# Kernel tuning notes

Hardware: AMD Instinct MI355X
Metric: run time of the kernel (lower is better)

## Reference

```python
import jax, jax.numpy as jnp
import numpy as np

B, S, D, H = 2, 2048, 1024, 16
HD = D // H


def setup_inputs() -> dict:
    key = jax.random.key(0)
    ks = jax.random.split(key, 6)
    scale = D ** -0.5
    return {
        "x": jax.random.normal(ks[0], (B, S, D), dtype=jnp.float32),
        "attn_mask": jnp.ones((B, S), dtype=bool),
        "wq": jax.random.normal(ks[1], (D, D), dtype=jnp.float32) * scale,
        "wk": jax.random.normal(ks[2], (D, D), dtype=jnp.float32) * scale,
        "wv": jax.random.normal(ks[3], (D, D), dtype=jnp.float32) * scale,
        "wo": jax.random.normal(ks[4], (D, D), dtype=jnp.float32) * scale,
        "bo": jax.random.normal(ks[5], (D,), dtype=jnp.float32) * 0.01,
    }


def reference(x, attn_mask, wq, wk, wv, wo, bo):
    b, s, d = x.shape
    # torch Linear: y = x @ W.T
    q = (x @ wq.T).reshape(b, s, H, HD).transpose(0, 2, 1, 3)  # (b,h,s,hd)
    k = (x @ wk.T).reshape(b, s, H, HD).transpose(0, 2, 1, 3)
    v = (x @ wv.T).reshape(b, s, H, HD).transpose(0, 2, 1, 3)
    scores = jnp.einsum("bhqd,bhkd->bhqk", q, k) * (HD ** -0.5)
    causal = jnp.triu(jnp.ones((s, s), dtype=bool), k=1)  # True above diagonal
    mask = causal[None, None, :, :] | (~attn_mask)[:, None, None, :]
    mask_value = jnp.finfo(scores.dtype).min / 2
    scores = jnp.where(mask, mask_value, scores)
    att = jax.nn.softmax(scores, axis=-1)
    ctx = jnp.einsum("bhqk,bhkd->bhqd", att, v)
    ctx = ctx.transpose(0, 2, 1, 3).reshape(b, s, d)
    return ctx @ wo.T + bo
```

## Files before the change

kernel.cpp:

```cpp
#include <hip/hip_runtime.h>
#include <stdint.h>

#define SEQ   2048
#define DMODEL 1024
#define NHEAD 16
#define HDIM  64
#define MTOT  4096

typedef short s16x8 __attribute__((ext_vector_type(8)));
typedef float f32x4 __attribute__((ext_vector_type(4)));
typedef float f32x16 __attribute__((ext_vector_type(16)));
typedef unsigned u32x4 __attribute__((ext_vector_type(4)));

#define LOG2E 1.44269504088896340736f

#if __has_builtin(__builtin_amdgcn_exp2f)
#define EXP2(x) __builtin_amdgcn_exp2f(x)
#else
#define EXP2(x) exp2f(x)
#endif

#define WAITV0 asm volatile("s_waitcnt vmcnt(0)" ::: "memory")
#define WAITV3 asm volatile("s_waitcnt vmcnt(3)" ::: "memory")
#define WAITV4 asm volatile("s_waitcnt vmcnt(4)" ::: "memory")

__device__ __forceinline__ short f2bf(float f) {
  union { float f; unsigned u; } v; v.f = f;
  unsigned u = v.u + 0x7fff + ((v.u >> 16) & 1);
  return (short)(u >> 16);
}

__device__ __forceinline__ void async_cp16(const void* g, void* l) {
  __builtin_amdgcn_global_load_lds(
      (const __attribute__((address_space(1))) void*)g,
      (__attribute__((address_space(3))) void*)l, 16, 0, 0);
}

__device__ __forceinline__ f32x4 mfma16(s16x8 a, s16x8 b, f32x4 c) {
  return __builtin_amdgcn_mfma_f32_16x16x32_bf16(a, b, c, 0, 0, 0);
}
__device__ __forceinline__ f32x16 mfma32(s16x8 a, s16x8 b, f32x16 c) {
  return __builtin_amdgcn_mfma_f32_32x32x16_bf16(a, b, c, 0, 0, 0);
}

__device__ __forceinline__ void plane32swap(unsigned& a, unsigned& b) {
#if __has_builtin(__builtin_amdgcn_permlane32_swap)
  auto r = __builtin_amdgcn_permlane32_swap(a, b, false, false);
  a = r[0]; b = r[1];
#else
  asm("v_permlane32_swap_b32 %0, %1" : "+v"(a), "+v"(b));
#endif
}

__global__ __launch_bounds__(256) void cast_kernel(
    const float* __restrict__ x,  const float* __restrict__ wq,
    const float* __restrict__ wk, const float* __restrict__ wv,
    const float* __restrict__ wo,
    short* __restrict__ xb,  short* __restrict__ wqb,
    short* __restrict__ wkb, short* __restrict__ wvb, short* __restrict__ wob) {
  int i = blockIdx.x * 256 + threadIdx.x;
  const float4* src; short* dst; int off;
  const int XN = 1 << 20, WN = 1 << 18;
  if (i < XN)            { src = (const float4*)x;  dst = xb;  off = i; }
  else if (i < XN + WN)  { src = (const float4*)wq; dst = wqb; off = i - XN; }
  else if (i < XN + 2*WN){ src = (const float4*)wk; dst = wkb; off = i - XN - WN; }
  else if (i < XN + 3*WN){ src = (const float4*)wv; dst = wvb; off = i - XN - 2*WN; }
  else                   { src = (const float4*)wo; dst = wob; off = i - XN - 3*WN; }
  float4 v = src[off];
  short4 o; o.x = f2bf(v.x); o.y = f2bf(v.y); o.z = f2bf(v.z); o.w = f2bf(v.w);
  *(short4*)(dst + off * 4) = o;
}

__global__ __launch_bounds__(512, 2) void qkv_gemm(
    const short* __restrict__ xb,  const short* __restrict__ wqb,
    const short* __restrict__ wkb, const short* __restrict__ wvb,
    short* __restrict__ Q, short* __restrict__ K, short* __restrict__ Vt) {
  __shared__ short SMEM[49152];
  short (*Abuf)[4096] = reinterpret_cast<short (*)[4096]>(SMEM);
  short (*Bbuf)[3][4096] = reinterpret_cast<short (*)[3][4096]>(SMEM + 3 * 4096);
  const int tid = threadIdx.x;
  const int w = tid >> 6, lane = tid & 63;
  const int c = lane & 15, g = lane >> 4;
  const int wm = w >> 2, wn = w & 3;
  const int n0 = blockIdx.x * 128, m0 = blockIdx.y * 128;
  const int srow = lane >> 2, schunk = lane & 3;

  f32x4 acc[3][4][2] = {};

#define QKV_STAGE(KT, BS)                                                      \
  {                                                                            \
    async_cp16(xb + (m0 + w * 16 + srow) * 1024 + (KT) * 32 + schunk * 8,      \
               &Abuf[BS][w * 512]);                                            \
    async_cp16(wqb + (n0 + w * 16 + srow) * 1024 + (KT) * 32 + schunk * 8,     \
               &Bbuf[BS][0][w * 512]);                                         \
    async_cp16(wkb + (n0 + w * 16 + srow) * 1024 + (KT) * 32 + schunk * 8,     \
               &Bbuf[BS][1][w * 512]);                                         \
    async_cp16(wvb + (n0 + w * 16 + srow) * 1024 + (KT) * 32 + schunk * 8,     \
               &Bbuf[BS][2][w * 512]);                                         \
  }

  QKV_STAGE(0, 0)
  QKV_STAGE(1, 1)
  for (int kt = 0; kt < 32; ++kt) {
    if (kt < 31) { WAITV4; } else { WAITV0; }
    __builtin_amdgcn_s_barrier();
    if (kt + 2 < 32) { QKV_STAGE(kt + 2, (kt + 2) % 3) }
    const int cur = kt % 3;
    s16x8 a[4];
#pragma unroll
    for (int t = 0; t < 4; ++t)
      a[t] = *(const s16x8*)&Abuf[cur][(wm * 64 + t * 16 + c) * 32 + g * 8];
#pragma unroll
    for (int z = 0; z < 3; ++z) {
      s16x8 b[2];
#pragma unroll
      for (int u = 0; u < 2; ++u)
        b[u] = *(const s16x8*)&Bbuf[cur][z][(wn * 32 + u * 16 + c) * 32 + g * 8];
      __builtin_amdgcn_s_setprio(1);
#pragma unroll
      for (int t = 0; t < 4; ++t)
#pragma unroll
        for (int u = 0; u < 2; ++u)
          acc[z][t][u] = mfma16(a[t], b[u], acc[z][t][u]);
      __builtin_amdgcn_s_setprio(0);
    }
  }

  short* E = SMEM;
  const int b0 = m0 >> 11, sbase = m0 & 2047, hgb = n0 >> 6;

#pragma unroll
  for (int z = 0; z < 3; ++z) {
    __syncthreads();
    if (z == 2) {
#pragma unroll
      for (int t = 0; t < 4; ++t)
#pragma unroll
        for (int u = 0; u < 2; ++u) {
          int col = wn * 32 + u * 16 + c;
          int m = wm * 64 + t * 16 + g * 4;
          int phys = (m >> 3) ^ (col & 15);
          short4 o;
          o.x = f2bf(acc[z][t][u][0]); o.y = f2bf(acc[z][t][u][1]);
          o.z = f2bf(acc[z][t][u][2]); o.w = f2bf(acc[z][t][u][3]);
          *(short4*)&E[col * 128 + phys * 8 + (m & 7)] = o;
        }
      __syncthreads();
#pragma unroll
      for (int p = 0; p < 4; ++p) {
        int R = p * 32 + (tid >> 4);
        int j = tid & 15;
        int phys = j ^ (R & 15);
        s16x8 v = *(const s16x8*)&E[R * 128 + phys * 8];
        int hloc = R >> 6, hd = R & 63;
        *(s16x8*)&Vt[(((b0 * 16 + hgb + hloc) * 64 + hd) * 2048) + sbase + j * 8] = v;
      }
    } else {
      const float scale = (z == 0) ? 0.125f * LOG2E : 1.0f;
#pragma unroll
      for (int t = 0; t < 4; ++t)
#pragma unroll
        for (int u = 0; u < 2; ++u)
#pragma unroll
          for (int r = 0; r < 4; ++r) {
            int m = wm * 64 + t * 16 + g * 4 + r;
            int col = wn * 32 + u * 16 + c;
            int phys = (col >> 3) ^ ((m >> 2) & 15);
            E[m * 128 + phys * 8 + (col & 7)] = f2bf(acc[z][t][u][r] * scale);
          }
      __syncthreads();
      short* __restrict__ dst = (z == 0) ? Q : K;
#pragma unroll
      for (int p = 0; p < 4; ++p) {
        int R = p * 64 + (tid >> 3);
        int j = tid & 7;
        int m = R >> 1, hloc = R & 1;
        int phys = (hloc * 8 + j) ^ ((m >> 2) & 15);
        s16x8 v = *(const s16x8*)&E[m * 128 + phys * 8];
        *(s16x8*)&dst[(((b0 * 16 + hgb + hloc) * 2048) + sbase + m) * 64 + j * 8] = v;
      }
    }
  }
}

#define STAGE_KV(T, BS)                                                        \
  _Pragma("unroll") for (int jj = 0; jj < 2; ++jj) {                           \
    int seg = qs * 2 + jj, sub = seg >> 2, pp = seg & 3;                       \
    async_cp16(Kg + ((T) * 64 + pp * 16 + srow) * 64 + sub * 32 + sw8,         \
               &Kbuf[p][BS][sub][pp * 512]);                                   \
    async_cp16(Vg + (pp * 16 + srow) * 2048 + (T) * 64 + sub * 32 + sw8,       \
               &Vlds[p][BS][sub][pp * 512]);                                   \
  }

__global__ __launch_bounds__(512, 4) void attn_kernel(
    const short* __restrict__ Q, const short* __restrict__ K,
    const short* __restrict__ Vt, short* __restrict__ ctx) {
  __shared__ __align__(16) short Kbuf[2][2][2][64 * 32];
  __shared__ __align__(16) short Vlds[2][2][2][64 * 32];
  __shared__ float Llds[2][4][32];

  const int tid = threadIdx.x;
  const int w = tid >> 6, lane = tid & 63;
  const int n31 = lane & 31, h = lane >> 5;
  const int p = w >> 2, qs = w & 3;
  const int bh = blockIdx.x;
  int bx = blockIdx.y;
  if (bx >= 8) bx = 23 - bx;
  const int qbase = bx * 128 + qs * 32;
  const short* __restrict__ Qg = Q + bh * (SEQ * HDIM);
  const short* __restrict__ Kg = K + bh * (SEQ * HDIM);
  const short* __restrict__ Vg = Vt + bh * (SEQ * HDIM);
  const int srow = lane >> 2, schunk = lane & 3;
  const int sw8 = (schunk ^ ((srow >> 1) & 3)) * 8;
  const int rsw = (n31 >> 1) & 3;

  s16x8 qf[4];
#pragma unroll
  for (int ch = 0; ch < 4; ++ch)
    qf[ch] = *(const s16x8*)&Qg[(qbase + n31) * 64 + ch * 16 + h * 8];

  float l_run = 0.f;
  f32x16 oacc[2] = {};

  const int qlo = qbase;
  STAGE_KV(p, 0)
  for (int j = 0; j <= bx; ++j) {
    __syncthreads();
    if (j < bx) { STAGE_KV(2 * (j + 1) + p, (j + 1) & 1) }

    const short (*Kc)[64 * 32] = Kbuf[p][j & 1];
    const short (*Vc)[64 * 32] = Vlds[p][j & 1];
    const int kbase = (2 * j + p) * 64;

    unsigned pk[2][8];
#pragma unroll
    for (int mt = 0; mt < 2; ++mt) {
      const int dk = qlo - (kbase + mt * 32);
      if (dk < 0) continue;
      f32x16 st = {};
      __builtin_amdgcn_s_setprio(1);
#pragma unroll
      for (int ch = 0; ch < 4; ++ch) {
        s16x8 ka = *(const s16x8*)
            &Kc[ch >> 1][(mt * 32 + n31) * 32 + ((((ch & 1) * 2 + h) ^ rsw) * 8)];
        st = mfma32(ka, qf[ch], st);
      }
      __builtin_amdgcn_s_setprio(0);
      if (dk == 0) {
#pragma unroll
        for (int reg = 0; reg < 16; ++reg) {
          int krow = (reg & 3) + 8 * (reg >> 2) + 4 * h;
          if (krow > n31) st[reg] = -1e30f;
        }
      }
#pragma unroll
      for (int i = 0; i < 8; ++i) {
        float p0 = EXP2(st[2 * i]);
        float p1 = EXP2(st[2 * i + 1]);
        unsigned u0 = __float_as_uint(p0);
        unsigned u1 = __float_as_uint(p1);
        l_run += __uint_as_float(u0 & 0xffff0000u);
        l_run += __uint_as_float(u1 & 0xffff0000u);
        pk[mt][i] = __builtin_amdgcn_perm(u1, u0, 0x07060302u);
      }
    }

#pragma unroll
    for (int mt = 0; mt < 2; ++mt) {
      if (qlo - (kbase + mt * 32) < 0) continue;
#pragma unroll
      for (int kb2 = 0; kb2 < 2; ++kb2) {
        const int kb = mt * 2 + kb2;
        unsigned q0 = pk[mt][kb2 * 4 + 0], q1 = pk[mt][kb2 * 4 + 1];
        unsigned q2 = pk[mt][kb2 * 4 + 2], q3 = pk[mt][kb2 * 4 + 3];
        plane32swap(q0, q2);
        plane32swap(q1, q3);
        u32x4 av; av.x = q0; av.y = q1; av.z = q2; av.w = q3;
        s16x8 pa = __builtin_bit_cast(s16x8, av);
        __builtin_amdgcn_s_setprio(1);
#pragma unroll
        for (int u = 0; u < 2; ++u) {
          s16x8 vf = *(const s16x8*)
              &Vc[kb >> 1][(u * 32 + n31) * 32 + ((((kb & 1) * 2 + h) ^ rsw) * 8)];
          oacc[u] = mfma32(pa, vf, oacc[u]);
        }
        __builtin_amdgcn_s_setprio(0);
      }
    }
  }

  __syncthreads();
  float lf = l_run + __shfl_xor(l_run, 32);
  float* Ocmb = reinterpret_cast<float*>(&Kbuf[0][0][0][0]);
  if (p == 1) {
#pragma unroll
    for (int rc = 0; rc < 8; ++rc) {
      f32x4 o4;
      o4[0] = oacc[rc >> 2][(rc & 3) * 4 + 0];
      o4[1] = oacc[rc >> 2][(rc & 3) * 4 + 1];
      o4[2] = oacc[rc >> 2][(rc & 3) * 4 + 2];
      o4[3] = oacc[rc >> 2][(rc & 3) * 4 + 3];
      *(f32x4*)&Ocmb[qs * 2048 + lane * 32 + ((rc ^ (lane & 7)) << 2)] = o4;
    }
    if (h == 0) Llds[1][qs][n31] = lf;
  }
  __syncthreads();
  if (p == 0) {
#pragma unroll
    for (int rc = 0; rc < 8; ++rc) {
      f32x4 o4 = *(const f32x4*)
          &Ocmb[qs * 2048 + lane * 32 + ((rc ^ (lane & 7)) << 2)];
      oacc[rc >> 2][(rc & 3) * 4 + 0] += o4[0];
      oacc[rc >> 2][(rc & 3) * 4 + 1] += o4[1];
      oacc[rc >> 2][(rc & 3) * 4 + 2] += o4[2];
      oacc[rc >> 2][(rc & 3) * 4 + 3] += o4[3];
    }
    float lt = lf + Llds[1][qs][n31];
    if (h == 0) Llds[0][qs][n31] = lt;
    float inv[4][4];
#pragma unroll
    for (int gi = 0; gi < 4; ++gi) {
      float4 lv = *(const float4*)&Llds[0][qs][gi * 8 + 4 * h];
      inv[gi][0] = 1.0f / lv.x; inv[gi][1] = 1.0f / lv.y;
      inv[gi][2] = 1.0f / lv.z; inv[gi][3] = 1.0f / lv.w;
    }
    const int b = bh >> 4, hh = bh & 15;
#pragma unroll
    for (int u = 0; u < 2; ++u)
#pragma unroll
      for (int gi = 0; gi < 4; ++gi)
#pragma unroll
        for (int ri = 0; ri < 4; ++ri) {
          int q = qbase + 8 * gi + 4 * h + ri;
          int hd = u * 32 + n31;
          ctx[(b * 2048 + q) * 1024 + hh * 64 + hd] =
              f2bf(oacc[u][gi * 4 + ri] * inv[gi][ri]);
        }
  }
}

__global__ __launch_bounds__(256) void out_gemm(
    const short* __restrict__ ctx, const short* __restrict__ wob,
    const float* __restrict__ bo, float* __restrict__ out) {
  __shared__ short Abuf[3][128 * 32];
  __shared__ short Bbuf[3][64 * 32];
  const int tid = threadIdx.x;
  const int w = tid >> 6, lane = tid & 63;
  const int c = lane & 15, g = lane >> 4;
  const int wm = w >> 1, wn = w & 1;
  const int n0 = blockIdx.y * 64, m0 = blockIdx.x * 128;
  const int srow = lane >> 2, schunk = lane & 3;

  f32x4 acc[4][2] = {};

#define OUT_STAGE(KT, BS)                                                      \
  {                                                                            \
    _Pragma("unroll") for (int j = 0; j < 2; ++j) {                            \
      int pp = w * 2 + j;                                                      \
      async_cp16(ctx + (m0 + pp * 16 + srow) * 1024 + (KT) * 32 + schunk * 8,  \
                 &Abuf[BS][pp * 512]);                                         \
    }                                                                          \
    async_cp16(wob + (n0 + w * 16 + srow) * 1024 + (KT) * 32 + schunk * 8,     \
               &Bbuf[BS][w * 512]);                                            \
  }

  OUT_STAGE(0, 0)
  OUT_STAGE(1, 1)
  for (int kt = 0; kt < 32; ++kt) {
    if (kt < 31) { WAITV3; } else { WAITV0; }
    __builtin_amdgcn_s_barrier();
    if (kt + 2 < 32) { OUT_STAGE(kt + 2, (kt + 2) % 3) }
    const int cur = kt % 3;
    s16x8 a[4], b[2];
#pragma unroll
    for (int t = 0; t < 4; ++t)
      a[t] = *(const s16x8*)&Abuf[cur][(wm * 64 + t * 16 + c) * 32 + g * 8];
#pragma unroll
    for (int u = 0; u < 2; ++u)
      b[u] = *(const s16x8*)&Bbuf[cur][(wn * 32 + u * 16 + c) * 32 + g * 8];
    __builtin_amdgcn_s_setprio(1);
#pragma unroll
    for (int t = 0; t < 4; ++t)
#pragma unroll
      for (int u = 0; u < 2; ++u)
        acc[t][u] = mfma16(a[t], b[u], acc[t][u]);
    __builtin_amdgcn_s_setprio(0);
  }

#pragma unroll
  for (int t = 0; t < 4; ++t)
#pragma unroll
    for (int u = 0; u < 2; ++u) {
      int col = n0 + wn * 32 + u * 16 + c;
      float bias = bo[col];
#pragma unroll
      for (int r = 0; r < 4; ++r) {
        int m = m0 + wm * 64 + t * 16 + g * 4 + r;
        out[m * 1024 + col] = acc[t][u][r] + bias;
      }
    }
}

extern "C" void kernel_launch(void* const* d_in, const int* in_sizes, int n_in,
                              void* d_out, int out_size, void* d_ws, size_t ws_size,
                              hipStream_t stream) {
  const float* x  = (const float*)d_in[0];
  const float* wq = (const float*)d_in[2];
  const float* wk = (const float*)d_in[3];
  const float* wv = (const float*)d_in[4];
  const float* wo = (const float*)d_in[5];
  const float* bo = (const float*)d_in[6];

  char* ws = (char*)d_ws;
  short* xb  = (short*)(ws);
  short* wqb = (short*)(ws + (size_t)( 8 << 20));
  short* wkb = (short*)(ws + (size_t)(10 << 20));
  short* wvb = (short*)(ws + (size_t)(12 << 20));
  short* wob = (short*)(ws + (size_t)(14 << 20));
  short* Qb  = (short*)(ws + (size_t)(16 << 20));
  short* Kb  = (short*)(ws + (size_t)(24 << 20));
  short* Vtb = (short*)(ws + (size_t)(32 << 20));
  short* ctx = (short*)(ws + (size_t)(40 << 20));
  float* out = (float*)d_out;

  cast_kernel<<<dim3(8192), dim3(256), 0, stream>>>(x, wq, wk, wv, wo,
                                                    xb, wqb, wkb, wvb, wob);
  qkv_gemm<<<dim3(8, 32), dim3(512), 0, stream>>>(xb, wqb, wkb, wvb,
                                                  Qb, Kb, Vtb);
  attn_kernel<<<dim3(32, 16), dim3(512), 0, stream>>>(Qb, Kb, Vtb, ctx);
  out_gemm<<<dim3(32, 16), dim3(256), 0, stream>>>(ctx, wob, bo, out);
}
```

Baseline: 169.7 us.

## Halve QKV GEMM tile width, double-buffer, and split attention epilogue across wave groups

The QKV projection GEMM now uses 128x64 tiles (one head per block) with a 2-stage double buffer instead of a 3-stage pipeline. This shrinks LDS and accumulator registers so occupancy can rise to 4 blocks per CU, and the grid doubles to 512 blocks. In exchange it loses prefetch depth and uses a full syncthreads each k-step. The attention epilogue now splits the cross-wave reduction so each wave group combines and writes half of the head dimension, balancing work that was previously done by one group only.

After: 172.3 us. About the same (+1.6%).

```diff
diff --git a/kernel.cpp b/kernel.cpp
--- a/kernel.cpp
+++ b/kernel.cpp
@@ -22,7 +22,6 @@
 
 #define WAITV0 asm volatile("s_waitcnt vmcnt(0)" ::: "memory")
 #define WAITV3 asm volatile("s_waitcnt vmcnt(3)" ::: "memory")
-#define WAITV4 asm volatile("s_waitcnt vmcnt(4)" ::: "memory")
 
 __device__ __forceinline__ short f2bf(float f) {
   union { float f; unsigned u; } v; v.f = f;
@@ -71,45 +70,43 @@
   *(short4*)(dst + off * 4) = o;
 }
 
-__global__ __launch_bounds__(512, 2) void qkv_gemm(
+__global__ __launch_bounds__(512, 4) void qkv_gemm(
     const short* __restrict__ xb,  const short* __restrict__ wqb,
     const short* __restrict__ wkb, const short* __restrict__ wvb,
     short* __restrict__ Q, short* __restrict__ K, short* __restrict__ Vt) {
-  __shared__ short SMEM[49152];
-  short (*Abuf)[4096] = reinterpret_cast<short (*)[4096]>(SMEM);
-  short (*Bbuf)[3][4096] = reinterpret_cast<short (*)[3][4096]>(SMEM + 3 * 4096);
+  __shared__ short Abuf[2][4096];
+  __shared__ short Bbuf[2][3][2048];
   const int tid = threadIdx.x;
   const int w = tid >> 6, lane = tid & 63;
   const int c = lane & 15, g = lane >> 4;
-  const int wm = w >> 2, wn = w & 3;
-  const int n0 = blockIdx.x * 128, m0 = blockIdx.y * 128;
+  const int wm = w >> 1, wn = w & 1;
+  const int n0 = blockIdx.x * 64, m0 = blockIdx.y * 128;
   const int srow = lane >> 2, schunk = lane & 3;
-
-  f32x4 acc[3][4][2] = {};
+  const short* wsel1 = (w < 4) ? wqb : wkb;
+  const int q1 = w & 3;
+
+  f32x4 acc[3][2][2] = {};
 
 #define QKV_STAGE(KT, BS)                                                      \
   {                                                                            \
     async_cp16(xb + (m0 + w * 16 + srow) * 1024 + (KT) * 32 + schunk * 8,      \
                &Abuf[BS][w * 512]);                                            \
-    async_cp16(wqb + (n0 + w * 16 + srow) * 1024 + (KT) * 32 + schunk * 8,     \
-               &Bbuf[BS][0][w * 512]);                                         \
-    async_cp16(wkb + (n0 + w * 16 + srow) * 1024 + (KT) * 32 + schunk * 8,     \
-               &Bbuf[BS][1][w * 512]);                                         \
-    async_cp16(wvb + (n0 + w * 16 + srow) * 1024 + (KT) * 32 + schunk * 8,     \
-               &Bbuf[BS][2][w * 512]);                                         \
+    async_cp16(wsel1 + (n0 + q1 * 16 + srow) * 1024 + (KT) * 32 + schunk * 8,  \
+               &Bbuf[BS][w >> 2][q1 * 512]);                                   \
+    if (w < 4)                                                                 \
+      async_cp16(wvb + (n0 + w * 16 + srow) * 1024 + (KT) * 32 + schunk * 8,   \
+                 &Bbuf[BS][2][w * 512]);                                       \
   }
 
   QKV_STAGE(0, 0)
-  QKV_STAGE(1, 1)
   for (int kt = 0; kt < 32; ++kt) {
-    if (kt < 31) { WAITV4; } else { WAITV0; }
-    __builtin_amdgcn_s_barrier();
-    if (kt + 2 < 32) { QKV_STAGE(kt + 2, (kt + 2) % 3) }
-    const int cur = kt % 3;
-    s16x8 a[4];
-#pragma unroll
-    for (int t = 0; t < 4; ++t)
-      a[t] = *(const s16x8*)&Abuf[cur][(wm * 64 + t * 16 + c) * 32 + g * 8];
+    __syncthreads();
+    if (kt + 1 < 32) { QKV_STAGE(kt + 1, (kt + 1) & 1) }
+    const int cur = kt & 1;
+    s16x8 a[2];
+#pragma unroll
+    for (int t = 0; t < 2; ++t)
+      a[t] = *(const s16x8*)&Abuf[cur][(wm * 32 + t * 16 + c) * 32 + g * 8];
 #pragma unroll
     for (int z = 0; z < 3; ++z) {
       s16x8 b[2];
@@ -118,7 +115,7 @@
         b[u] = *(const s16x8*)&Bbuf[cur][z][(wn * 32 + u * 16 + c) * 32 + g * 8];
       __builtin_amdgcn_s_setprio(1);
 #pragma unroll
-      for (int t = 0; t < 4; ++t)
+      for (int t = 0; t < 2; ++t)
 #pragma unroll
         for (int u = 0; u < 2; ++u)
           acc[z][t][u] = mfma16(a[t], b[u], acc[z][t][u]);
@@ -126,58 +123,56 @@
     }
   }
 
-  short* E = SMEM;
-  const int b0 = m0 >> 11, sbase = m0 & 2047, hgb = n0 >> 6;
+  short* E = &Abuf[0][0];
+  const int b0 = m0 >> 11, sbase = m0 & 2047, hgb = blockIdx.x;
 
 #pragma unroll
   for (int z = 0; z < 3; ++z) {
     __syncthreads();
     if (z == 2) {
 #pragma unroll
-      for (int t = 0; t < 4; ++t)
+      for (int t = 0; t < 2; ++t)
 #pragma unroll
         for (int u = 0; u < 2; ++u) {
           int col = wn * 32 + u * 16 + c;
-          int m = wm * 64 + t * 16 + g * 4;
+          int m = wm * 32 + t * 16 + g * 4;
           int phys = (m >> 3) ^ (col & 15);
           short4 o;
-          o.x = f2bf(acc[z][t][u][0]); o.y = f2bf(acc[z][t][u][1]);
-          o.z = f2bf(acc[z][t][u][2]); o.w = f2bf(acc[z][t][u][3]);
+          o.x = f2bf(acc[2][t][u][0]); o.y = f2bf(acc[2][t][u][1]);
+          o.z = f2bf(acc[2][t][u][2]); o.w = f2bf(acc[2][t][u][3]);
           *(short4*)&E[col * 128 + phys * 8 + (m & 7)] = o;
         }
       __syncthreads();
 #pragma unroll
-      for (int p = 0; p < 4; ++p) {
-        int R = p * 32 + (tid >> 4);
-        int j = tid & 15;
+      for (int p2 = 0; p2 < 2; ++p2) {
+        int idx = p2 * 512 + tid;
+        int R = idx >> 4, j = idx & 15;
         int phys = j ^ (R & 15);
         s16x8 v = *(const s16x8*)&E[R * 128 + phys * 8];
-        int hloc = R >> 6, hd = R & 63;
-        *(s16x8*)&Vt[(((b0 * 16 + hgb + hloc) * 64 + hd) * 2048) + sbase + j * 8] = v;
+        *(s16x8*)&Vt[((b0 * 16 + hgb) * 64 + R) * 2048 + sbase + j * 8] = v;
       }
     } else {
       const float scale = (z == 0) ? 0.125f * LOG2E : 1.0f;
 #pragma unroll
-      for (int t = 0; t < 4; ++t)
+      for (int t = 0; t < 2; ++t)
 #pragma unroll
         for (int u = 0; u < 2; ++u)
 #pragma unroll
           for (int r = 0; r < 4; ++r) {
-            int m = wm * 64 + t * 16 + g * 4 + r;
+            int m = wm * 32 + t * 16 + g * 4 + r;
             int col = wn * 32 + u * 16 + c;
-            int phys = (col >> 3) ^ ((m >> 2) & 15);
-            E[m * 128 + phys * 8 + (col & 7)] = f2bf(acc[z][t][u][r] * scale);
+            int phys = (col >> 3) ^ ((m >> 2) & 7);
+            E[m * 64 + phys * 8 + (col & 7)] = f2bf(acc[z][t][u][r] * scale);
           }
       __syncthreads();
       short* __restrict__ dst = (z == 0) ? Q : K;
 #pragma unroll
-      for (int p = 0; p < 4; ++p) {
-        int R = p * 64 + (tid >> 3);
-        int j = tid & 7;
-        int m = R >> 1, hloc = R & 1;
-        int phys = (hloc * 8 + j) ^ ((m >> 2) & 15);
-        s16x8 v = *(const s16x8*)&E[m * 128 + phys * 8];
-        *(s16x8*)&dst[(((b0 * 16 + hgb + hloc) * 2048) + sbase + m) * 64 + j * 8] = v;
+      for (int p2 = 0; p2 < 2; ++p2) {
+        int idx = p2 * 512 + tid;
+        int m = idx >> 3, j = idx & 7;
+        int phys = j ^ ((m >> 2) & 7);
+        s16x8 v = *(const s16x8*)&E[m * 64 + phys * 8];
+        *(s16x8*)&dst[((b0 * 16 + hgb) * 2048 + sbase + m) * 64 + j * 8] = v;
       }
     }
   }
@@ -197,7 +192,7 @@
     const short* __restrict__ Vt, short* __restrict__ ctx) {
   __shared__ __align__(16) short Kbuf[2][2][2][64 * 32];
   __shared__ __align__(16) short Vlds[2][2][2][64 * 32];
-  __shared__ float Llds[2][4][32];
+  __shared__ float Llds[3][4][32];
 
   const int tid = threadIdx.x;
   const int w = tid >> 6, lane = tid & 63;
@@ -292,58 +287,81 @@
   __syncthreads();
   float lf = l_run + __shfl_xor(l_run, 32);
   float* Ocmb = reinterpret_cast<float*>(&Kbuf[0][0][0][0]);
+  if (h == 0) Llds[p][qs][n31] = lf;
   if (p == 1) {
 #pragma unroll
-    for (int rc = 0; rc < 8; ++rc) {
+    for (int rc = 0; rc < 4; ++rc) {
       f32x4 o4;
-      o4[0] = oacc[rc >> 2][(rc & 3) * 4 + 0];
-      o4[1] = oacc[rc >> 2][(rc & 3) * 4 + 1];
-      o4[2] = oacc[rc >> 2][(rc & 3) * 4 + 2];
-      o4[3] = oacc[rc >> 2][(rc & 3) * 4 + 3];
+      o4[0] = oacc[0][rc * 4 + 0]; o4[1] = oacc[0][rc * 4 + 1];
+      o4[2] = oacc[0][rc * 4 + 2]; o4[3] = oacc[0][rc * 4 + 3];
       *(f32x4*)&Ocmb[qs * 2048 + lane * 32 + ((rc ^ (lane & 7)) << 2)] = o4;
     }
-    if (h == 0) Llds[1][qs][n31] = lf;
+  } else {
+#pragma unroll
+    for (int rc2 = 0; rc2 < 4; ++rc2) {
+      f32x4 o4;
+      o4[0] = oacc[1][rc2 * 4 + 0]; o4[1] = oacc[1][rc2 * 4 + 1];
+      o4[2] = oacc[1][rc2 * 4 + 2]; o4[3] = oacc[1][rc2 * 4 + 3];
+      *(f32x4*)&Ocmb[qs * 2048 + lane * 32 + (((rc2 + 4) ^ (lane & 7)) << 2)] = o4;
+    }
   }
   __syncthreads();
   if (p == 0) {
 #pragma unroll
-    for (int rc = 0; rc < 8; ++rc) {
+    for (int rc = 0; rc < 4; ++rc) {
       f32x4 o4 = *(const f32x4*)
           &Ocmb[qs * 2048 + lane * 32 + ((rc ^ (lane & 7)) << 2)];
-      oacc[rc >> 2][(rc & 3) * 4 + 0] += o4[0];
-      oacc[rc >> 2][(rc & 3) * 4 + 1] += o4[1];
-      oacc[rc >> 2][(rc & 3) * 4 + 2] += o4[2];
-      oacc[rc >> 2][(rc & 3) * 4 + 3] += o4[3];
-    }
-    float lt = lf + Llds[1][qs][n31];
-    if (h == 0) Llds[0][qs][n31] = lt;
+      oacc[0][rc * 4 + 0] += o4[0]; oacc[0][rc * 4 + 1] += o4[1];
+      oacc[0][rc * 4 + 2] += o4[2]; oacc[0][rc * 4 + 3] += o4[3];
+    }
+  } else {
+#pragma unroll
+    for (int rc2 = 0; rc2 < 4; ++rc2) {
+      f32x4 o4 = *(const f32x4*)
+          &Ocmb[qs * 2048 + lane * 32 + (((rc2 + 4) ^ (lane & 7)) << 2)];
+      oacc[1][rc2 * 4 + 0] += o4[0]; oacc[1][rc2 * 4 + 1] += o4[1];
+      oacc[1][rc2 * 4 + 2] += o4[2]; oacc[1][rc2 * 4 + 3] += o4[3];
+    }
+  }
+  float lt = lf + Llds[1 - p][qs][n31];
+  if (p == 0 && h == 0) Llds[2][qs][n31] = lt;
+  __syncthreads();
+  {
     float inv[4][4];
 #pragma unroll
     for (int gi = 0; gi < 4; ++gi) {
-      float4 lv = *(const float4*)&Llds[0][qs][gi * 8 + 4 * h];
+      float4 lv = *(const float4*)&Llds[2][qs][gi * 8 + 4 * h];
       inv[gi][0] = 1.0f / lv.x; inv[gi][1] = 1.0f / lv.y;
       inv[gi][2] = 1.0f / lv.z; inv[gi][3] = 1.0f / lv.w;
     }
     const int b = bh >> 4, hh = bh & 15;
-#pragma unroll
-    for (int u = 0; u < 2; ++u)
+    if (p == 0) {
 #pragma unroll
       for (int gi = 0; gi < 4; ++gi)
 #pragma unroll
         for (int ri = 0; ri < 4; ++ri) {
           int q = qbase + 8 * gi + 4 * h + ri;
-          int hd = u * 32 + n31;
-          ctx[(b * 2048 + q) * 1024 + hh * 64 + hd] =
-              f2bf(oacc[u][gi * 4 + ri] * inv[gi][ri]);
+          ctx[(b * 2048 + q) * 1024 + hh * 64 + n31] =
+              f2bf(oacc[0][gi * 4 + ri] * inv[gi][ri]);
         }
+    } else {
+#pragma unroll
+      for (int gi = 0; gi < 4; ++gi)
+#pragma unroll
+        for (int ri = 0; ri < 4; ++ri) {
+          int q = qbase + 8 * gi + 4 * h + ri;
+          ctx[(b * 2048 + q) * 1024 + hh * 64 + 32 + n31] =
+              f2bf(oacc[1][gi * 4 + ri] * inv[gi][ri]);
+        }
+    }
   }
 }
 
 __global__ __launch_bounds__(256) void out_gemm(
     const short* __restrict__ ctx, const short* __restrict__ wob,
     const float* __restrict__ bo, float* __restrict__ out) {
-  __shared__ short Abuf[3][128 * 32];
-  __shared__ short Bbuf[3][64 * 32];
+  __shared__ short OAbuf[3][128 * 32];
+  __shared__ short OBbuf[3][64 * 32];
   const int tid = threadIdx.x;
   const int w = tid >> 6, lane = tid & 63;
   const int c = lane & 15, g = lane >> 4;
@@ -358,10 +376,10 @@
     _Pragma("unroll") for (int j = 0; j < 2; ++j) {                            \
       int pp = w * 2 + j;                                                      \
       async_cp16(ctx + (m0 + pp * 16 + srow) * 1024 + (KT) * 32 + schunk * 8,  \
-                 &Abuf[BS][pp * 512]);                                         \
+                 &OAbuf[BS][pp * 512]);                                        \
     }                                                                          \
     async_cp16(wob + (n0 + w * 16 + srow) * 1024 + (KT) * 32 + schunk * 8,     \
-               &Bbuf[BS][w * 512]);                                            \
+               &OBbuf[BS][w * 512]);                                           \
   }
 
   OUT_STAGE(0, 0)
@@ -374,10 +392,10 @@
     s16x8 a[4], b[2];
 #pragma unroll
     for (int t = 0; t < 4; ++t)
-      a[t] = *(const s16x8*)&Abuf[cur][(wm * 64 + t * 16 + c) * 32 + g * 8];
+      a[t] = *(const s16x8*)&OAbuf[cur][(wm * 64 + t * 16 + c) * 32 + g * 8];
 #pragma unroll
     for (int u = 0; u < 2; ++u)
-      b[u] = *(const s16x8*)&Bbuf[cur][(wn * 32 + u * 16 + c) * 32 + g * 8];
+      b[u] = *(const s16x8*)&OBbuf[cur][(wn * 32 + u * 16 + c) * 32 + g * 8];
     __builtin_amdgcn_s_setprio(1);
 #pragma unroll
     for (int t = 0; t < 4; ++t)
@@ -425,8 +443,8 @@
 
   cast_kernel<<<dim3(8192), dim3(256), 0, stream>>>(x, wq, wk, wv, wo,
                                                     xb, wqb, wkb, wvb, wob);
-  qkv_gemm<<<dim3(8, 32), dim3(512), 0, stream>>>(xb, wqb, wkb, wvb,
-                                                  Qb, Kb, Vtb);
+  qkv_gemm<<<dim3(16, 32), dim3(512), 0, stream>>>(xb, wqb, wkb, wvb,
+                                                   Qb, Kb, Vtb);
   attn_kernel<<<dim3(32, 16), dim3(512), 0, stream>>>(Qb, Kb, Vtb, ctx);
   out_gemm<<<dim3(32, 16), dim3(256), 0, stream>>>(ctx, wob, bo, out);
 }
```
